# Performance work log

Hardware: AMD Instinct MI355X
Metric: run time of the kernel (lower is better)

Reference implementation:

```python
import jax, jax.numpy as jnp
import numpy as np

LMAX = 5
RESOLUTION = 12
ASPECT_RATIO = 2
BATCH = 256
NB = 2 * RESOLUTION                       # res_beta = 24
NA = round(2 * ASPECT_RATIO * RESOLUTION)  # res_alpha = res_gamma = 48
DIM = sum((2 * l + 1) ** 2 for l in range(LMAX + 1))  # 286

# normalize2mom constant for tanh: (E_{z~N(0,1)}[tanh(z)^2])^{-1/2}
_x = np.linspace(-12.0, 12.0, 1_000_001)
_pdf = np.exp(-0.5 * _x * _x) / np.sqrt(2.0 * np.pi)
ACT_CST = float(np.trapz(np.tanh(_x) ** 2 * _pdf, _x) ** -0.5)  # ~1.5927


def _su2_generators(j):
    m = np.arange(-j, j)
    raising = np.diag(-np.sqrt(j * (j + 1) - m * (m + 1)), k=-1).astype(complex)
    m = np.arange(-j + 1, j + 1)
    lowering = np.diag(np.sqrt(j * (j + 1) - m * (m - 1)), k=1).astype(complex)
    m = np.arange(-j, j + 1)
    return np.stack([0.5 * (raising + lowering), np.diag(1j * m), -0.5j * (raising - lowering)])


def _q_real_to_complex(l):
    q = np.zeros((2 * l + 1, 2 * l + 1), dtype=complex)
    for m in range(-l, 0):
        q[l + m, l + abs(m)] = 1 / np.sqrt(2)
        q[l + m, l - abs(m)] = -1j / np.sqrt(2)
    q[l, l] = 1
    for m in range(1, l + 1):
        q[l + m, l + abs(m)] = (-1) ** m / np.sqrt(2)
        q[l + m, l - abs(m)] = 1j * (-1) ** m / np.sqrt(2)
    return (-1j) ** l * q


def _so3_generators(l):
    X = _su2_generators(l)
    Q = _q_real_to_complex(l)
    return np.real(np.conj(Q.T)[None] @ X @ Q[None])  # real [3, 2l+1, 2l+1]


def _expm_angles(A, t):
    """exp(t_n * A) for real antisymmetric A via eigendecomposition. -> [n, d, d] real"""
    vals, vecs = np.linalg.eig(A.astype(complex))
    inv = np.linalg.inv(vecs)
    phases = np.exp(t[:, None] * vals[None, :])  # [n, d]
    return np.real(np.einsum('ij,nj,jk->nik', vecs, phases, inv))


def _build_D_and_qw():
    # Euler angle grids (e3nn SO3Grid convention)
    b = (np.arange(NB) + 0.5) / NB * np.pi          # beta   [nb]
    a = np.arange(NA) / NA * 2.0 * np.pi            # alpha=gamma [na]
    blocks = []
    for l in range(LMAX + 1):
        X = _so3_generators(l)
        Ra = _expm_angles(X[1], a)   # exp(alpha * X1)  [na,d,d]
        Rb = _expm_angles(X[0], b)   # exp(beta  * X0)  [nb,d,d]
        # D^l(a,b,c) = Ra[a] @ Rb[b] @ Ra[c]
        Dl = np.einsum('xij,yjk,zkl->xyzil', Ra, Rb, Ra)
        blocks.append(np.sqrt(2 * l + 1) * Dl.reshape(NA, NB, NA, -1))
    D = np.concatenate(blocks, axis=-1).astype(np.float32)  # [na, nb, na, dim]
    # lie_learn / Kostelec-Rockmore quadrature weights for beta
    bb = NB // 2
    k = np.arange(bb)
    j = np.arange(2 * bb)
    w = (2.0 / bb) * np.sin(np.pi * (2 * j + 1) / (4.0 * bb)) * np.sum(
        (1.0 / (2 * k + 1))[None, :]
        * np.sin((2 * j[:, None] + 1) * (2 * k[None, :] + 1) * np.pi / (4.0 * bb)),
        axis=1,
    )
    w = w / (2.0 * (2 * bb) ** 2)
    qw = (w * NB ** 2 / NA ** 2).astype(np.float32)  # [nb]
    return jnp.asarray(D), jnp.asarray(qw)


def setup_inputs() -> dict:
    key = jax.random.key(0)
    features = jax.random.normal(key, (BATCH, DIM), dtype=jnp.float32)
    D, qw = _build_D_and_qw()
    return {"features": features, "D": D, "qw": qw}


def reference(features, D, qw):
    dim = D.shape[-1]
    s = jnp.sqrt(jnp.asarray(dim, features.dtype))
    # to_grid: [B, dim] x [na, nb, na, dim] -> [B, na, nb, na]
    g = jnp.einsum('bi,xyzi->bxyz', features, D) / s
    # normalized pointwise nonlinearity on SO(3) samples
    g = ACT_CST * jnp.tanh(g)
    # from_grid: quadrature-weighted projection back onto flat Wigner basis
    return jnp.einsum('bxyz,y,xyzi->bi', g, qw, D) * s
```

## Files before the change

### kernel.cpp

```cpp
#include <hip/hip_runtime.h>
#include <hip/hip_bf16.h>

#define DIM    286
#define DIMP   288
#define NBATCH 256
#define NB_    24
#define NA_    48
#define ZC     32
#define NTILES 1728
#define NCHUNK 256
#define S_CONST 16.911534525287763f
#define INV_S   0.05913123959890826f
#define ACT_CST 1.5927f
#define TWO_LOG2E 2.8853900817779268f

typedef short bf16x8 __attribute__((ext_vector_type(8)));
typedef float f32x4  __attribute__((ext_vector_type(4)));

#define WS_FBF  0u
#define WS_PART 147456u

typedef const __attribute__((address_space(1))) char GA;
typedef __attribute__((address_space(3))) char LA;
__device__ __forceinline__ void gload_lds16(const void* g, void* l) {
    __builtin_amdgcn_global_load_lds((GA*)g, (LA*)l, 16, 0, 0);
}

__global__ void k_prepF(const float* __restrict__ F, __hip_bfloat16* __restrict__ Fbf) {
    int o = blockIdx.x * 256 + threadIdx.x;
    int row = o / DIMP, col = o % DIMP;
    float v = (col < DIM) ? F[row * DIM + col] * INV_S : 0.f;
    Fbf[o] = __float2bfloat16(v);
}

__launch_bounds__(512, 2)
__global__ void k_main(const __hip_bfloat16* __restrict__ Fbf,
                       const float* __restrict__ D,
                       const float* __restrict__ qw,
                       __hip_bfloat16* __restrict__ part) {
    __shared__ __align__(16) float Traw[2][9216];
    __shared__ __align__(16) char DsB[18432];
    __shared__ __align__(16) char DtB[18432];
    __shared__ __align__(16) char GsB[16384];
    __shared__ float qs[24];

    int t = threadIdx.x;
    int wave = t >> 6, lane = t & 63, ln = lane & 15, q = lane >> 4;
    int cA = (ln * 64 + q * 16) ^ ((ln & 7) << 4);
    int rq = ln * 64 + q * 16;
    int gA0 = (wave << 11) + (rq ^ ((ln >> 2) << 4));
    int gA1 = (wave << 11) + 1024 + (rq ^ ((4 + (ln >> 2)) << 4));

    if (t < 24) qs[t] = qw[t] * S_CONST;

    int rowbase = wave * 32;
    const __hip_bfloat16* fp0 = Fbf + (size_t)(rowbase + ln) * DIMP + q * 8;
    const __hip_bfloat16* fp1 = fp0 + 16 * DIMP;

    f32x4 acc[2][18];
    #pragma unroll
    for (int h = 0; h < 2; ++h)
        #pragma unroll
        for (int n = 0; n < 18; ++n) acc[h][n] = (f32x4){0.f, 0.f, 0.f, 0.f};

    int bx = blockIdx.x;
    int tstart = (bx < 192) ? bx * 7 : bx * 6 + 192;
    int ntile = (bx < 192) ? 7 : 6;

    int zseed = t / 144, iseed = t % 144;

    #define STAGE(TI, BUF) do {                                                    \
        const char* _s = (const char*)(D + (size_t)(tstart + (TI)) * 9152);        \
        char* _d = (char*)Traw[BUF];                                               \
        _Pragma("unroll")                                                          \
        for (int _j = 0; _j < 5; ++_j) {                                           \
            int _c = wave + _j * 8;                                                \
            if (_c < 35 || (_c == 35 && lane < 48))                                \
                gload_lds16(_s + _c * 1024 + lane * 16, _d + _c * 1024);           \
        }                                                                          \
    } while (0)

    STAGE(0, 0);
    STAGE(1, 1);
    asm volatile("s_waitcnt lgkmcnt(0)" ::: "memory");

    #pragma unroll 1
    for (int k = 0; k < ntile; ++k) {
        if (k + 1 < ntile) {
            if (wave < 4) asm volatile("s_waitcnt vmcnt(5)" ::: "memory");
            else          asm volatile("s_waitcnt vmcnt(4)" ::: "memory");
        } else {
            asm volatile("s_waitcnt vmcnt(0)" ::: "memory");
        }
        __builtin_amdgcn_s_barrier();

        const float* T = Traw[k & 1];
        {
            int zz = zseed, ii = iseed;
            #pragma unroll
            for (int m = 0; m < 9; ++m) {
                int i = ii * 2;
                __hip_bfloat162 o2;
                if (i < DIM) {
                    float2 v = *(const float2*)(&T[zz * DIM + i]);
                    o2.x = __float2bfloat16(v.x); o2.y = __float2bfloat16(v.y);
                } else {
                    o2.x = __float2bfloat16(0.f); o2.y = o2.x;
                }
                int off = (((i >> 5) * 2048) + zz * 64 + (i & 31) * 2) ^ ((zz & 7) << 4);
                *(__hip_bfloat162*)(DsB + off) = o2;
                zz += 3; ii += 80;
                if (ii >= 144) { ii -= 144; ++zz; }
            }
        }
        #pragma unroll
        for (int s5 = 0; s5 < 3; ++s5) {
            int idx = t + s5 * 512;
            if (idx < 1152) {
                int i = idx >> 2, zc = idx & 3;
                __hip_bfloat16 o8[8];
                #pragma unroll
                for (int j = 0; j < 8; ++j)
                    o8[j] = __float2bfloat16(T[(zc * 8 + j) * DIM + i]);
                int off = (i * 64 + zc * 16) ^ ((i & 7) << 4);
                *(bf16x8*)(DtB + off) = *(const bf16x8*)o8;
            }
        }
        asm volatile("s_waitcnt lgkmcnt(0)" ::: "memory");
        __builtin_amdgcn_s_barrier();

        if (k + 2 < ntile) STAGE(k + 2, k & 1);

        int z0t = (tstart + k) * 32;
        float qv0 = qs[((z0t + ln) / 48) % 24];
        float qv1 = qs[((z0t + 16 + ln) / 48) % 24];

        f32x4 g00 = (f32x4){0.f,0.f,0.f,0.f}, g01 = (f32x4){0.f,0.f,0.f,0.f};
        f32x4 g10 = (f32x4){0.f,0.f,0.f,0.f}, g11 = (f32x4){0.f,0.f,0.f,0.f};
        #pragma unroll 3
        for (int ks = 0; ks < 9; ++ks) {
            bf16x8 a0 = *(const bf16x8*)(fp0 + ks * 32);
            bf16x8 a1 = *(const bf16x8*)(fp1 + ks * 32);
            bf16x8 b0 = *(const bf16x8*)(DsB + ks * 2048 + cA);
            bf16x8 b1 = *(const bf16x8*)(DsB + ks * 2048 + 1024 + cA);
            g00 = __builtin_amdgcn_mfma_f32_16x16x32_bf16(a0, b0, g00, 0, 0, 0);
            g01 = __builtin_amdgcn_mfma_f32_16x16x32_bf16(a0, b1, g01, 0, 0, 0);
            g10 = __builtin_amdgcn_mfma_f32_16x16x32_bf16(a1, b0, g10, 0, 0, 0);
            g11 = __builtin_amdgcn_mfma_f32_16x16x32_bf16(a1, b1, g11, 0, 0, 0);
        }
        #pragma unroll
        for (int h = 0; h < 2; ++h) {
            #pragma unroll
            for (int zh = 0; zh < 2; ++zh) {
                f32x4 g = (h == 0) ? (zh == 0 ? g00 : g01) : (zh == 0 ? g10 : g11);
                float qv = (zh == 0) ? qv0 : qv1;
                #pragma unroll
                for (int r = 0; r < 4; ++r) {
                    float x = g[r];
                    float a = fabsf(x);
                    float e = __builtin_amdgcn_exp2f(-TWO_LOG2E * a);
                    float v = ACT_CST - 2.f * ACT_CST * e * __builtin_amdgcn_rcpf(1.f + e);
                    v = copysignf(v, x) * qv;
                    int row = h * 16 + q * 4 + r;
                    int goff = (wave << 11)
                             + ((row * 64 + (zh * 16 + ln) * 2) ^ ((row >> 2) << 4));
                    *(__hip_bfloat16*)(GsB + goff) = __float2bfloat16(v);
                }
            }
        }
        bf16x8 a20 = *(const bf16x8*)(GsB + gA0);
        bf16x8 a21 = *(const bf16x8*)(GsB + gA1);
        #pragma unroll
        for (int nf = 0; nf < 18; ++nf) {
            bf16x8 b2 = *(const bf16x8*)(DtB + nf * 1024 + cA);
            acc[0][nf] = __builtin_amdgcn_mfma_f32_16x16x32_bf16(a20, b2, acc[0][nf], 0, 0, 0);
            acc[1][nf] = __builtin_amdgcn_mfma_f32_16x16x32_bf16(a21, b2, acc[1][nf], 0, 0, 0);
        }
        __builtin_amdgcn_s_barrier();
    }
    #undef STAGE

    __hip_bfloat16* pw = part + (size_t)bx * (NBATCH * DIMP) + (size_t)rowbase * DIMP;
    #pragma unroll
    for (int h = 0; h < 2; ++h) {
        #pragma unroll
        for (int m = 0; m < 9; ++m) {
            __hip_bfloat16 o8[8];
            #pragma unroll
            for (int j = 0; j < 8; ++j)
                o8[j] = __float2bfloat16(acc[h][2 * m + (j >> 2)][j & 3]);
            *(bf16x8*)(pw + (size_t)((h * 9 + m) * 64 + lane) * 8) = *(const bf16x8*)o8;
        }
    }
}

__global__ void k_reduce(const __hip_bfloat16* __restrict__ part, float* __restrict__ out) {
    __shared__ float red[3][16][8];
    int t = threadIdx.x, wave = t >> 6, lane = t & 63;
    int j = lane & 15;
    int zg = wave * 4 + (lane >> 4);
    int s = blockIdx.x * 16 + j;
    const __hip_bfloat16* p = part + (size_t)s * 8;
    float sum[8];
    #pragma unroll
    for (int kk = 0; kk < 8; ++kk) sum[kk] = 0.f;
    #pragma unroll 4
    for (int ii = 0; ii < 16; ++ii) {
        bf16x8 v = *(const bf16x8*)(p + (size_t)(zg * 16 + ii) * (NBATCH * DIMP));
        #pragma unroll
        for (int kk = 0; kk < 8; ++kk) {
            __hip_bfloat16 h; *(short*)&h = v[kk];
            sum[kk] += __bfloat162float(h);
        }
    }
    #pragma unroll
    for (int kk = 0; kk < 8; ++kk) {
        sum[kk] += __shfl_down(sum[kk], 16);
        sum[kk] += __shfl_down(sum[kk], 32);
    }
    if (wave > 0 && lane < 16) {
        #pragma unroll
        for (int kk = 0; kk < 8; ++kk) red[wave - 1][lane][kk] = sum[kk];
    }
    __syncthreads();
    if (wave == 0 && lane < 16) {
        #pragma unroll
        for (int w = 0; w < 3; ++w)
            #pragma unroll
            for (int kk = 0; kk < 8; ++kk) sum[kk] += red[w][lane][kk];
        int wr = s / 1152, si = s % 1152;
        int lane_m = si % 64, m9 = si / 64;
        int h = m9 / 9, m = m9 % 9, q = lane_m >> 4, ln = lane_m & 15;
        int rowb = wr * 32 + h * 16 + q * 4;
        #pragma unroll
        for (int j8 = 0; j8 < 8; ++j8) {
            int nf = 2 * m + (j8 >> 2), r = j8 & 3;
            int i = nf * 16 + ln;
            if (i < DIM) out[(rowb + r) * DIM + i] = sum[j8];
        }
    }
}

extern "C" void kernel_launch(void* const* d_in, const int* in_sizes, int n_in,
                              void* d_out, int out_size, void* d_ws, size_t ws_size,
                              hipStream_t stream) {
    const float* F  = (const float*)d_in[0];
    const float* D  = (const float*)d_in[1];
    const float* qw = (const float*)d_in[2];
    char* ws = (char*)d_ws;
    __hip_bfloat16* Fbf = (__hip_bfloat16*)(ws + WS_FBF);
    __hip_bfloat16* part = (__hip_bfloat16*)(ws + WS_PART);

    k_prepF<<<288, 256, 0, stream>>>(F, Fbf);
    k_main<<<NCHUNK, 512, 0, stream>>>(Fbf, D, qw, part);
    k_reduce<<<576, 256, 0, stream>>>(part, (float*)d_out);
}
```

Before: 138.6 us.

## Double-buffer bf16 D tiles and overlap conversion with MFMA phases

The bf16 converted D buffers (DsB/DtB) are now double-buffered, so the fp32-to-bf16 conversion for the next tile is interleaved between the MFMA phases of the current tile instead of running in a separate serialized stage. The second GEMM is split into two halves that reuse a smaller per-wave G scratch, which halves GsB. One barrier per iteration goes away, and the conversion's LDS and VALU work can hide behind matrix-core work. In exchange, LDS use grows by about 28 KB per block, which may hurt 2-blocks-per-CU occupancy. The wait on the next staged tile now uses a full vmcnt(0) rather than a partial count.

```diff
diff --git a/kernel.cpp b/kernel.cpp
--- a/kernel.cpp
+++ b/kernel.cpp
@@ -39,17 +39,15 @@
                        const float* __restrict__ qw,
                        __hip_bfloat16* __restrict__ part) {
     __shared__ __align__(16) float Traw[2][9216];
-    __shared__ __align__(16) char DsB[18432];
-    __shared__ __align__(16) char DtB[18432];
-    __shared__ __align__(16) char GsB[16384];
+    __shared__ __align__(16) char DsB[2][18432];
+    __shared__ __align__(16) char DtB[2][18432];
+    __shared__ __align__(16) char GsB[8192];
     __shared__ float qs[24];
 
     int t = threadIdx.x;
     int wave = t >> 6, lane = t & 63, ln = lane & 15, q = lane >> 4;
     int cA = (ln * 64 + q * 16) ^ ((ln & 7) << 4);
-    int rq = ln * 64 + q * 16;
-    int gA0 = (wave << 11) + (rq ^ ((ln >> 2) << 4));
-    int gA1 = (wave << 11) + 1024 + (rq ^ ((4 + (ln >> 2)) << 4));
+    int gA = (wave << 10) + ((ln * 64 + q * 16) ^ ((ln >> 2) << 4));
 
     if (t < 24) qs[t] = qw[t] * S_CONST;
 
@@ -80,56 +78,65 @@
         }                                                                          \
     } while (0)
 
+    #define CONV_DS(TBUF, DBUF) do {                                               \
+        const float* _T = Traw[TBUF];                                              \
+        char* _Ds = DsB[DBUF];                                                     \
+        int zz = zseed, ii = iseed;                                                \
+        _Pragma("unroll")                                                          \
+        for (int m = 0; m < 9; ++m) {                                              \
+            int i = ii * 2;                                                        \
+            __hip_bfloat162 o2;                                                    \
+            if (i < DIM) {                                                         \
+                float2 v = *(const float2*)(&_T[zz * DIM + i]);                    \
+                o2.x = __float2bfloat16(v.x); o2.y = __float2bfloat16(v.y);        \
+            } else {                                                               \
+                o2.x = __float2bfloat16(0.f); o2.y = o2.x;                         \
+            }                                                                      \
+            int off = (((i >> 5) * 2048) + zz * 64 + (i & 31) * 2) ^ ((zz & 7) << 4); \
+            *(__hip_bfloat162*)(_Ds + off) = o2;                                   \
+            zz += 3; ii += 80;                                                     \
+            if (ii >= 144) { ii -= 144; ++zz; }                                    \
+        }                                                                          \
+    } while (0)
+
+    #define CONV_DT(TBUF, DBUF) do {                                               \
+        const float* _T = Traw[TBUF];                                              \
+        char* _Dt = DtB[DBUF];                                                     \
+        _Pragma("unroll")                                                          \
+        for (int s5 = 0; s5 < 3; ++s5) {                                           \
+            int idx = t + s5 * 512;                                                \
+            if (idx < 1152) {                                                      \
+                int i = idx >> 2, zc = idx & 3;                                    \
+                __hip_bfloat16 o8[8];                                              \
+                _Pragma("unroll")                                                  \
+                for (int j = 0; j < 8; ++j)                                        \
+                    o8[j] = __float2bfloat16(_T[(zc * 8 + j) * DIM + i]);          \
+                int off = (i * 64 + zc * 16) ^ ((i & 7) << 4);                     \
+                *(bf16x8*)(_Dt + off) = *(const bf16x8*)o8;                        \
+            }                                                                      \
+        }                                                                          \
+    } while (0)
+
     STAGE(0, 0);
+    asm volatile("s_waitcnt vmcnt(0) lgkmcnt(0)" ::: "memory");
+    __builtin_amdgcn_s_barrier();
     STAGE(1, 1);
+    CONV_DS(0, 0);
+    CONV_DT(0, 0);
     asm volatile("s_waitcnt lgkmcnt(0)" ::: "memory");
+    __builtin_amdgcn_s_barrier();
 
     #pragma unroll 1
     for (int k = 0; k < ntile; ++k) {
-        if (k + 1 < ntile) {
-            if (wave < 4) asm volatile("s_waitcnt vmcnt(5)" ::: "memory");
-            else          asm volatile("s_waitcnt vmcnt(4)" ::: "memory");
-        } else {
+        int cur = k & 1, nxt = cur ^ 1;
+        bool more = (k + 1 < ntile);
+        if (more) {
             asm volatile("s_waitcnt vmcnt(0)" ::: "memory");
-        }
-        __builtin_amdgcn_s_barrier();
-
-        const float* T = Traw[k & 1];
-        {
-            int zz = zseed, ii = iseed;
-            #pragma unroll
-            for (int m = 0; m < 9; ++m) {
-                int i = ii * 2;
-                __hip_bfloat162 o2;
-                if (i < DIM) {
-                    float2 v = *(const float2*)(&T[zz * DIM + i]);
-                    o2.x = __float2bfloat16(v.x); o2.y = __float2bfloat16(v.y);
-                } else {
-                    o2.x = __float2bfloat16(0.f); o2.y = o2.x;
-                }
-                int off = (((i >> 5) * 2048) + zz * 64 + (i & 31) * 2) ^ ((zz & 7) << 4);
-                *(__hip_bfloat162*)(DsB + off) = o2;
-                zz += 3; ii += 80;
-                if (ii >= 144) { ii -= 144; ++zz; }
-            }
-        }
-        #pragma unroll
-        for (int s5 = 0; s5 < 3; ++s5) {
-            int idx = t + s5 * 512;
-            if (idx < 1152) {
-                int i = idx >> 2, zc = idx & 3;
-                __hip_bfloat16 o8[8];
-                #pragma unroll
-                for (int j = 0; j < 8; ++j)
-                    o8[j] = __float2bfloat16(T[(zc * 8 + j) * DIM + i]);
-                int off = (i * 64 + zc * 16) ^ ((i & 7) << 4);
-                *(bf16x8*)(DtB + off) = *(const bf16x8*)o8;
-            }
-        }
-        asm volatile("s_waitcnt lgkmcnt(0)" ::: "memory");
-        __builtin_amdgcn_s_barrier();
-
-        if (k + 2 < ntile) STAGE(k + 2, k & 1);
+            __builtin_amdgcn_s_barrier();
+            if (k + 2 < ntile) STAGE(k + 2, cur);
+        }
+        const char* dsR = DsB[cur];
+        const char* dtR = DtB[cur];
 
         int z0t = (tstart + k) * 32;
         float qv0 = qs[((z0t + ln) / 48) % 24];
@@ -141,44 +148,76 @@
         for (int ks = 0; ks < 9; ++ks) {
             bf16x8 a0 = *(const bf16x8*)(fp0 + ks * 32);
             bf16x8 a1 = *(const bf16x8*)(fp1 + ks * 32);
-            bf16x8 b0 = *(const bf16x8*)(DsB + ks * 2048 + cA);
-            bf16x8 b1 = *(const bf16x8*)(DsB + ks * 2048 + 1024 + cA);
+            bf16x8 b0 = *(const bf16x8*)(dsR + ks * 2048 + cA);
+            bf16x8 b1 = *(const bf16x8*)(dsR + ks * 2048 + 1024 + cA);
             g00 = __builtin_amdgcn_mfma_f32_16x16x32_bf16(a0, b0, g00, 0, 0, 0);
             g01 = __builtin_amdgcn_mfma_f32_16x16x32_bf16(a0, b1, g01, 0, 0, 0);
             g10 = __builtin_amdgcn_mfma_f32_16x16x32_bf16(a1, b0, g10, 0, 0, 0);
             g11 = __builtin_amdgcn_mfma_f32_16x16x32_bf16(a1, b1, g11, 0, 0, 0);
         }
-        #pragma unroll
-        for (int h = 0; h < 2; ++h) {
-            #pragma unroll
-            for (int zh = 0; zh < 2; ++zh) {
-                f32x4 g = (h == 0) ? (zh == 0 ? g00 : g01) : (zh == 0 ? g10 : g11);
-                float qv = (zh == 0) ? qv0 : qv1;
-                #pragma unroll
-                for (int r = 0; r < 4; ++r) {
-                    float x = g[r];
-                    float a = fabsf(x);
-                    float e = __builtin_amdgcn_exp2f(-TWO_LOG2E * a);
-                    float v = ACT_CST - 2.f * ACT_CST * e * __builtin_amdgcn_rcpf(1.f + e);
-                    v = copysignf(v, x) * qv;
-                    int row = h * 16 + q * 4 + r;
-                    int goff = (wave << 11)
-                             + ((row * 64 + (zh * 16 + ln) * 2) ^ ((row >> 2) << 4));
-                    *(__hip_bfloat16*)(GsB + goff) = __float2bfloat16(v);
-                }
-            }
-        }
-        bf16x8 a20 = *(const bf16x8*)(GsB + gA0);
-        bf16x8 a21 = *(const bf16x8*)(GsB + gA1);
-        #pragma unroll
-        for (int nf = 0; nf < 18; ++nf) {
-            bf16x8 b2 = *(const bf16x8*)(DtB + nf * 1024 + cA);
-            acc[0][nf] = __builtin_amdgcn_mfma_f32_16x16x32_bf16(a20, b2, acc[0][nf], 0, 0, 0);
-            acc[1][nf] = __builtin_amdgcn_mfma_f32_16x16x32_bf16(a21, b2, acc[1][nf], 0, 0, 0);
-        }
-        __builtin_amdgcn_s_barrier();
+
+        if (more) CONV_DS(nxt, nxt);
+
+        #pragma unroll
+        for (int zh = 0; zh < 2; ++zh) {
+            f32x4 g = (zh == 0) ? g00 : g01;
+            float qv = (zh == 0) ? qv0 : qv1;
+            #pragma unroll
+            for (int r = 0; r < 4; ++r) {
+                float x = g[r];
+                float a = fabsf(x);
+                float e = __builtin_amdgcn_exp2f(-TWO_LOG2E * a);
+                float v = ACT_CST - 2.f * ACT_CST * e * __builtin_amdgcn_rcpf(1.f + e);
+                v = copysignf(v, x) * qv;
+                int goff = (wave << 10)
+                         + (((q * 4 + r) * 64 + (zh * 16 + ln) * 2) ^ (q << 4));
+                *(__hip_bfloat16*)(GsB + goff) = __float2bfloat16(v);
+            }
+        }
+        {
+            bf16x8 a20 = *(const bf16x8*)(GsB + gA);
+            #pragma unroll
+            for (int nf = 0; nf < 18; ++nf) {
+                bf16x8 b2 = *(const bf16x8*)(dtR + nf * 1024 + cA);
+                acc[0][nf] = __builtin_amdgcn_mfma_f32_16x16x32_bf16(a20, b2, acc[0][nf], 0, 0, 0);
+            }
+        }
+
+        if (more) CONV_DT(nxt, nxt);
+
+        #pragma unroll
+        for (int zh = 0; zh < 2; ++zh) {
+            f32x4 g = (zh == 0) ? g10 : g11;
+            float qv = (zh == 0) ? qv0 : qv1;
+            #pragma unroll
+            for (int r = 0; r < 4; ++r) {
+                float x = g[r];
+                float a = fabsf(x);
+                float e = __builtin_amdgcn_exp2f(-TWO_LOG2E * a);
+                float v = ACT_CST - 2.f * ACT_CST * e * __builtin_amdgcn_rcpf(1.f + e);
+                v = copysignf(v, x) * qv;
+                int goff = (wave << 10)
+                         + (((q * 4 + r) * 64 + (zh * 16 + ln) * 2) ^ (q << 4));
+                *(__hip_bfloat16*)(GsB + goff) = __float2bfloat16(v);
+            }
+        }
+        {
+            bf16x8 a21 = *(const bf16x8*)(GsB + gA);
+            #pragma unroll
+            for (int nf = 0; nf < 18; ++nf) {
+                bf16x8 b2 = *(const bf16x8*)(dtR + nf * 1024 + cA);
+                acc[1][nf] = __builtin_amdgcn_mfma_f32_16x16x32_bf16(a21, b2, acc[1][nf], 0, 0, 0);
+            }
+        }
+
+        if (more) {
+            asm volatile("s_waitcnt lgkmcnt(0)" ::: "memory");
+            __builtin_amdgcn_s_barrier();
+        }
     }
     #undef STAGE
+    #undef CONV_DS
+    #undef CONV_DT
 
     __hip_bfloat16* pw = part + (size_t)bx * (NBATCH * DIMP) + (size_t)rowbase * DIMP;
     #pragma unroll
```

New measurement: 138.6 us. No clear change (+0.0%).

## Fuse prep, main and reduce kernels into one cooperative kernel with grid syncs

Applied to the files above, without the earlier changes.

Merges the three launches (feature bf16 conversion, main grid projection, partial-sum reduction) into a single cooperative kernel that uses grid.sync between phases. The D tile staging is issued before the first grid sync so it overlaps with the feature conversion. The goal is to remove two kernel launch overheads and the inter-kernel gaps. The cost is two grid-wide barriers, and the reduction layout changes to 8 threads per output slot with shuffles instead of LDS.

```diff
diff --git a/kernel.cpp b/kernel.cpp
--- a/kernel.cpp
+++ b/kernel.cpp
@@ -1,5 +1,8 @@
 #include <hip/hip_runtime.h>
 #include <hip/hip_bf16.h>
+#include <hip/hip_cooperative_groups.h>
+
+namespace cg = cooperative_groups;
 
 #define DIM    286
 #define DIMP   288
@@ -26,23 +29,19 @@
     __builtin_amdgcn_global_load_lds((GA*)g, (LA*)l, 16, 0, 0);
 }
 
-__global__ void k_prepF(const float* __restrict__ F, __hip_bfloat16* __restrict__ Fbf) {
-    int o = blockIdx.x * 256 + threadIdx.x;
-    int row = o / DIMP, col = o % DIMP;
-    float v = (col < DIM) ? F[row * DIM + col] * INV_S : 0.f;
-    Fbf[o] = __float2bfloat16(v);
-}
-
 __launch_bounds__(512, 2)
-__global__ void k_main(const __hip_bfloat16* __restrict__ Fbf,
-                       const float* __restrict__ D,
-                       const float* __restrict__ qw,
-                       __hip_bfloat16* __restrict__ part) {
+__global__ void k_all(const float* __restrict__ F, const float* __restrict__ D,
+                      const float* __restrict__ qw,
+                      __hip_bfloat16* __restrict__ Fbf,
+                      __hip_bfloat16* __restrict__ part,
+                      float* __restrict__ out) {
     __shared__ __align__(16) float Traw[2][9216];
     __shared__ __align__(16) char DsB[18432];
     __shared__ __align__(16) char DtB[18432];
     __shared__ __align__(16) char GsB[16384];
     __shared__ float qs[24];
+
+    cg::grid_group grid = cg::this_grid();
 
     int t = threadIdx.x;
     int wave = t >> 6, lane = t & 63, ln = lane & 15, q = lane >> 4;
@@ -53,21 +52,9 @@
 
     if (t < 24) qs[t] = qw[t] * S_CONST;
 
-    int rowbase = wave * 32;
-    const __hip_bfloat16* fp0 = Fbf + (size_t)(rowbase + ln) * DIMP + q * 8;
-    const __hip_bfloat16* fp1 = fp0 + 16 * DIMP;
-
-    f32x4 acc[2][18];
-    #pragma unroll
-    for (int h = 0; h < 2; ++h)
-        #pragma unroll
-        for (int n = 0; n < 18; ++n) acc[h][n] = (f32x4){0.f, 0.f, 0.f, 0.f};
-
     int bx = blockIdx.x;
     int tstart = (bx < 192) ? bx * 7 : bx * 6 + 192;
     int ntile = (bx < 192) ? 7 : 6;
-
-    int zseed = t / 144, iseed = t % 144;
 
     #define STAGE(TI, BUF) do {                                                    \
         const char* _s = (const char*)(D + (size_t)(tstart + (TI)) * 9152);        \
@@ -82,7 +69,29 @@
 
     STAGE(0, 0);
     STAGE(1, 1);
-    asm volatile("s_waitcnt lgkmcnt(0)" ::: "memory");
+
+    {
+        int tid = bx * 512 + t;
+        if (tid < 73728) {
+            int row = tid / DIMP, col = tid % DIMP;
+            float v = (col < DIM) ? F[row * DIM + col] * INV_S : 0.f;
+            Fbf[tid] = __float2bfloat16(v);
+        }
+    }
+    __threadfence();
+    grid.sync();
+
+    int rowbase = wave * 32;
+    const __hip_bfloat16* fp0 = Fbf + (size_t)(rowbase + ln) * DIMP + q * 8;
+    const __hip_bfloat16* fp1 = fp0 + 16 * DIMP;
+
+    f32x4 acc[2][18];
+    #pragma unroll
+    for (int h = 0; h < 2; ++h)
+        #pragma unroll
+        for (int n = 0; n < 18; ++n) acc[h][n] = (f32x4){0.f, 0.f, 0.f, 0.f};
+
+    int zseed = t / 144, iseed = t % 144;
 
     #pragma unroll 1
     for (int k = 0; k < ntile; ++k) {
@@ -192,51 +201,45 @@
             *(bf16x8*)(pw + (size_t)((h * 9 + m) * 64 + lane) * 8) = *(const bf16x8*)o8;
         }
     }
-}
-
-__global__ void k_reduce(const __hip_bfloat16* __restrict__ part, float* __restrict__ out) {
-    __shared__ float red[3][16][8];
-    int t = threadIdx.x, wave = t >> 6, lane = t & 63;
-    int j = lane & 15;
-    int zg = wave * 4 + (lane >> 4);
-    int s = blockIdx.x * 16 + j;
-    const __hip_bfloat16* p = part + (size_t)s * 8;
-    float sum[8];
-    #pragma unroll
-    for (int kk = 0; kk < 8; ++kk) sum[kk] = 0.f;
-    #pragma unroll 4
-    for (int ii = 0; ii < 16; ++ii) {
-        bf16x8 v = *(const bf16x8*)(p + (size_t)(zg * 16 + ii) * (NBATCH * DIMP));
-        #pragma unroll
-        for (int kk = 0; kk < 8; ++kk) {
-            __hip_bfloat16 h; *(short*)&h = v[kk];
-            sum[kk] += __bfloat162float(h);
-        }
-    }
-    #pragma unroll
-    for (int kk = 0; kk < 8; ++kk) {
-        sum[kk] += __shfl_down(sum[kk], 16);
-        sum[kk] += __shfl_down(sum[kk], 32);
-    }
-    if (wave > 0 && lane < 16) {
-        #pragma unroll
-        for (int kk = 0; kk < 8; ++kk) red[wave - 1][lane][kk] = sum[kk];
-    }
-    __syncthreads();
-    if (wave == 0 && lane < 16) {
-        #pragma unroll
-        for (int w = 0; w < 3; ++w)
-            #pragma unroll
-            for (int kk = 0; kk < 8; ++kk) sum[kk] += red[w][lane][kk];
-        int wr = s / 1152, si = s % 1152;
-        int lane_m = si % 64, m9 = si / 64;
-        int h = m9 / 9, m = m9 % 9, q = lane_m >> 4, ln = lane_m & 15;
-        int rowb = wr * 32 + h * 16 + q * 4;
-        #pragma unroll
-        for (int j8 = 0; j8 < 8; ++j8) {
-            int nf = 2 * m + (j8 >> 2), r = j8 & 3;
-            int i = nf * 16 + ln;
-            if (i < DIM) out[(rowb + r) * DIM + i] = sum[j8];
+
+    __threadfence();
+    grid.sync();
+
+    {
+        int tid = bx * 512 + t;
+        if (tid < 73728) {
+            int s = tid >> 3, sub = tid & 7;
+            const __hip_bfloat16* p = part + (size_t)s * 8;
+            float sum[8];
+            #pragma unroll
+            for (int kk = 0; kk < 8; ++kk) sum[kk] = 0.f;
+            #pragma unroll 8
+            for (int ii = 0; ii < 32; ++ii) {
+                bf16x8 v = *(const bf16x8*)(p + (size_t)(sub * 32 + ii) * (NBATCH * DIMP));
+                #pragma unroll
+                for (int kk = 0; kk < 8; ++kk) {
+                    __hip_bfloat16 hh; *(short*)&hh = v[kk];
+                    sum[kk] += __bfloat162float(hh);
+                }
+            }
+            #pragma unroll
+            for (int kk = 0; kk < 8; ++kk) {
+                sum[kk] += __shfl_down(sum[kk], 4);
+                sum[kk] += __shfl_down(sum[kk], 2);
+                sum[kk] += __shfl_down(sum[kk], 1);
+            }
+            if (sub == 0) {
+                int wr = s / 1152, si = s % 1152;
+                int lane_m = si % 64, m9 = si / 64;
+                int h = m9 / 9, m = m9 % 9, qq = lane_m >> 4, lnn = lane_m & 15;
+                int rowb = wr * 32 + h * 16 + qq * 4;
+                #pragma unroll
+                for (int j8 = 0; j8 < 8; ++j8) {
+                    int nf = 2 * m + (j8 >> 2), r = j8 & 3;
+                    int i = nf * 16 + lnn;
+                    if (i < DIM) out[(rowb + r) * DIM + i] = sum[j8];
+                }
+            }
         }
     }
 }
@@ -248,10 +251,10 @@
     const float* D  = (const float*)d_in[1];
     const float* qw = (const float*)d_in[2];
     char* ws = (char*)d_ws;
-    __hip_bfloat16* Fbf = (__hip_bfloat16*)(ws + WS_FBF);
+    __hip_bfloat16* Fbf  = (__hip_bfloat16*)(ws + WS_FBF);
     __hip_bfloat16* part = (__hip_bfloat16*)(ws + WS_PART);
-
-    k_prepF<<<288, 256, 0, stream>>>(F, Fbf);
-    k_main<<<NCHUNK, 512, 0, stream>>>(Fbf, D, qw, part);
-    k_reduce<<<576, 256, 0, stream>>>(part, (float*)d_out);
+    float* outp = (float*)d_out;
+
+    void* args[] = {(void*)&F, (void*)&D, (void*)&qw, (void*)&Fbf, (void*)&part, (void*)&outp};
+    hipLaunchCooperativeKernel((const void*)k_all, dim3(NCHUNK), dim3(512), args, 0, stream);
 }
```

Result: slower. 338.6 us (+144.3%).

## Prefetch D tiles into registers instead of double-buffered LDS staging

Applied to the files above, without the earlier changes.

Replaces the async global-to-LDS double-buffered staging of raw fp32 D tiles with a register prefetch of the next tile, issued during compute of the current tile. This drops the 73KB Traw LDS buffer, which lowers LDS use and may allow higher occupancy. It also removes the end-of-iteration barrier and reduces unroll of the first GEMM loop. The cost is more registers per thread (25 floats), a prefetch depth of only one tile, and some strided global loads for the transposed copy. A tail of 128 threads does synchronous, uncoalesced global loads each iteration.

```diff
diff --git a/kernel.cpp b/kernel.cpp
--- a/kernel.cpp
+++ b/kernel.cpp
@@ -20,12 +20,6 @@
 #define WS_FBF  0u
 #define WS_PART 147456u
 
-typedef const __attribute__((address_space(1))) char GA;
-typedef __attribute__((address_space(3))) char LA;
-__device__ __forceinline__ void gload_lds16(const void* g, void* l) {
-    __builtin_amdgcn_global_load_lds((GA*)g, (LA*)l, 16, 0, 0);
-}
-
 __global__ void k_prepF(const float* __restrict__ F, __hip_bfloat16* __restrict__ Fbf) {
     int o = blockIdx.x * 256 + threadIdx.x;
     int row = o / DIMP, col = o % DIMP;
@@ -38,7 +32,6 @@
                        const float* __restrict__ D,
                        const float* __restrict__ qw,
                        __hip_bfloat16* __restrict__ part) {
-    __shared__ __align__(16) float Traw[2][9216];
     __shared__ __align__(16) char DsB[18432];
     __shared__ __align__(16) char DtB[18432];
     __shared__ __align__(16) char GsB[16384];
@@ -68,33 +61,35 @@
     int ntile = (bx < 192) ? 7 : 6;
 
     int zseed = t / 144, iseed = t % 144;
-
-    #define STAGE(TI, BUF) do {                                                    \
-        const char* _s = (const char*)(D + (size_t)(tstart + (TI)) * 9152);        \
-        char* _d = (char*)Traw[BUF];                                               \
+    int ti0 = t >> 2,        tz0 = t & 3;
+    int ti1 = (t + 512) >> 2, tz1 = (t + 512) & 3;
+
+    float2 sds[9];
+    float  sdt[16];
+
+    #define LOADT(TI) do {                                                         \
+        const float* Dp = D + (size_t)(tstart + (TI)) * 9152;                      \
+        int zz = zseed, ii = iseed;                                                \
         _Pragma("unroll")                                                          \
-        for (int _j = 0; _j < 5; ++_j) {                                           \
-            int _c = wave + _j * 8;                                                \
-            if (_c < 35 || (_c == 35 && lane < 48))                                \
-                gload_lds16(_s + _c * 1024 + lane * 16, _d + _c * 1024);           \
+        for (int m = 0; m < 9; ++m) {                                              \
+            if (ii * 2 < DIM) sds[m] = *(const float2*)(Dp + zz * DIM + ii * 2);   \
+            zz += 3; ii += 80;                               \
+            if (ii >= 144) { ii -= 144; ++zz; }                                    \
+        }                                                                          \
+        _Pragma("unroll")                                                          \
+        for (int j = 0; j < 8; ++j) {                                              \
+            sdt[j]     = Dp[(tz0 * 8 + j) * DIM + ti0];                            \
+            sdt[8 + j] = Dp[(tz1 * 8 + j) * DIM + ti1];                            \
         }                                                                          \
     } while (0)
 
-    STAGE(0, 0);
-    STAGE(1, 1);
-    asm volatile("s_waitcnt lgkmcnt(0)" ::: "memory");
+    LOADT(0);
 
     #pragma unroll 1
     for (int k = 0; k < ntile; ++k) {
-        if (k + 1 < ntile) {
-            if (wave < 4) asm volatile("s_waitcnt vmcnt(5)" ::: "memory");
-            else          asm volatile("s_waitcnt vmcnt(4)" ::: "memory");
-        } else {
-            asm volatile("s_waitcnt vmcnt(0)" ::: "memory");
-        }
+        asm volatile("s_waitcnt vmcnt(0)" ::: "memory");
         __builtin_amdgcn_s_barrier();
 
-        const float* T = Traw[k & 1];
         {
             int zz = zseed, ii = iseed;
             #pragma unroll
@@ -102,8 +97,8 @@
                 int i = ii * 2;
                 __hip_bfloat162 o2;
                 if (i < DIM) {
-                    float2 v = *(const float2*)(&T[zz * DIM + i]);
-                    o2.x = __float2bfloat16(v.x); o2.y = __float2bfloat16(v.y);
+                    o2.x = __float2bfloat16(sds[m].x);
+                    o2.y = __float2bfloat16(sds[m].y);
                 } else {
                     o2.x = __float2bfloat16(0.f); o2.y = o2.x;
                 }
@@ -113,23 +108,33 @@
                 if (ii >= 144) { ii -= 144; ++zz; }
             }
         }
-        #pragma unroll
-        for (int s5 = 0; s5 < 3; ++s5) {
-            int idx = t + s5 * 512;
-            if (idx < 1152) {
-                int i = idx >> 2, zc = idx & 3;
-                __hip_bfloat16 o8[8];
-                #pragma unroll
-                for (int j = 0; j < 8; ++j)
-                    o8[j] = __float2bfloat16(T[(zc * 8 + j) * DIM + i]);
-                int off = (i * 64 + zc * 16) ^ ((i & 7) << 4);
-                *(bf16x8*)(DtB + off) = *(const bf16x8*)o8;
-            }
+        {
+            __hip_bfloat16 o8[8];
+            #pragma unroll
+            for (int j = 0; j < 8; ++j) o8[j] = __float2bfloat16(sdt[j]);
+            int off0 = (ti0 * 64 + tz0 * 16) ^ ((ti0 & 7) << 4);
+            *(bf16x8*)(DtB + off0) = *(const bf16x8*)o8;
+            #pragma unroll
+            for (int j = 0; j < 8; ++j) o8[j] = __float2bfloat16(sdt[8 + j]);
+            int off1 = (ti1 * 64 + tz1 * 16) ^ ((ti1 & 7) << 4);
+            *(bf16x8*)(DtB + off1) = *(const bf16x8*)o8;
+        }
+        if (t < 128) {
+            const float* Dp = D + (size_t)(tstart + k) * 9152;
+            int idx = t + 1024;
+            int i = idx >> 2, zc = idx & 3;
+            __hip_bfloat16 o8[8];
+            #pragma unroll
+            for (int j = 0; j < 8; ++j)
+                o8[j] = __float2bfloat16(Dp[(zc * 8 + j) * DIM + i]);
+            int off = (i * 64 + zc * 16) ^ ((i & 7) << 4);
+            *(bf16x8*)(DtB + off) = *(const bf16x8*)o8;
         }
         asm volatile("s_waitcnt lgkmcnt(0)" ::: "memory");
         __builtin_amdgcn_s_barrier();
 
-        if (k + 2 < ntile) STAGE(k + 2, k & 1);
+        if (k + 1 < ntile) LOADT(k + 1);
+        asm volatile("" ::: "memory");
 
         int z0t = (tstart + k) * 32;
         float qv0 = qs[((z0t + ln) / 48) % 24];
@@ -137,7 +142,7 @@
 
         f32x4 g00 = (f32x4){0.f,0.f,0.f,0.f}, g01 = (f32x4){0.f,0.f,0.f,0.f};
         f32x4 g10 = (f32x4){0.f,0.f,0.f,0.f}, g11 = (f32x4){0.f,0.f,0.f,0.f};
-        #pragma unroll 3
+        #pragma unroll 2
         for (int ks = 0; ks < 9; ++ks) {
             bf16x8 a0 = *(const bf16x8*)(fp0 + ks * 32);
             bf16x8 a1 = *(const bf16x8*)(fp1 + ks * 32);
@@ -176,9 +181,8 @@
             acc[0][nf] = __builtin_amdgcn_mfma_f32_16x16x32_bf16(a20, b2, acc[0][nf], 0, 0, 0);
             acc[1][nf] = __builtin_amdgcn_mfma_f32_16x16x32_bf16(a21, b2, acc[1][nf], 0, 0, 0);
         }
-        __builtin_amdgcn_s_barrier();
-    }
-    #undef STAGE
+    }
+    #undef LOADT
 
     __hip_bfloat16* pw = part + (size_t)bx * (NBATCH * DIMP) + (size_t)rowbase * DIMP;
     #pragma unroll
```

Result: slower. 232.1 us (+67.5%).
